# Kernel tuning notes

Hardware: AMD Instinct MI355X
Metric: run time of the kernel (lower is better)

The kernel has to match this reference:

```python
import jax, jax.numpy as jnp
import numpy as np

REG_MAX = 16
BOX_W = 7.5
OBJ_W = 1.0
TOPK = 10
EPS = 1e-7


def dfl_decode(x, reg_max):
    # x: [B, 4*reg_max, N] -> expected value of per-side distribution -> [B, N, 4] (xyxy)
    B, C, N = x.shape
    x = x.reshape(B, 4, reg_max, N)
    p = jax.nn.softmax(x, axis=2)
    proj = jnp.arange(reg_max, dtype=x.dtype)
    return jnp.einsum('bkrn,r->bnk', p, proj)


def bbox_ciou(b1, b2):
    # b1: [B,N,1,4], b2: [B,1,M,4], xyxy -> [B,N,M]
    x11, y11, x12, y12 = b1[..., 0], b1[..., 1], b1[..., 2], b1[..., 3]
    x21, y21, x22, y22 = b2[..., 0], b2[..., 1], b2[..., 2], b2[..., 3]
    w1, h1 = x12 - x11, y12 - y11
    w2, h2 = x22 - x21, y22 - y21
    iw = jnp.clip(jnp.minimum(x12, x22) - jnp.maximum(x11, x21), 0.0)
    ih = jnp.clip(jnp.minimum(y12, y22) - jnp.maximum(y11, y21), 0.0)
    inter = iw * ih
    union = w1 * h1 + w2 * h2 - inter + EPS
    iou = inter / union
    cw = jnp.maximum(x12, x22) - jnp.minimum(x11, x21)
    ch = jnp.maximum(y12, y22) - jnp.minimum(y11, y21)
    c2 = cw * cw + ch * ch + EPS
    rho2 = ((x21 + x22 - x11 - x12) ** 2 + (y21 + y22 - y11 - y12) ** 2) * 0.25
    v = (4.0 / (np.pi ** 2)) * (jnp.arctan(w2 / (h2 + EPS)) - jnp.arctan(w1 / (h1 + EPS))) ** 2
    alpha = jax.lax.stop_gradient(v / (v - iou + 1.0 + EPS))
    return iou - rho2 / c2 - alpha * v


def setup_inputs() -> dict:
    key = jax.random.key(0)
    k1, k2, k3, k4 = jax.random.split(key, 4)
    B, N, M = 8, 34000, 64
    boxes = jax.random.normal(k1, (B, 4 * REG_MAX, N), dtype=jnp.float32)
    scores = jax.random.normal(k2, (B, N), dtype=jnp.float32)
    # GT boxes: valid xyxy in roughly the same [0, reg_max) range as decoded preds
    xy = jax.random.uniform(k3, (B, M, 2), dtype=jnp.float32) * 11.0
    wh = jax.random.uniform(k4, (B, M, 2), dtype=jnp.float32) * 4.0 + 0.5
    targets = jnp.concatenate([xy, xy + wh], axis=-1)
    return {'boxes': boxes, 'scores': scores, 'targets': targets}


def reference(boxes, scores, targets):
    B, N = scores.shape
    M = targets.shape[1]
    pb = dfl_decode(boxes, REG_MAX)                     # [B,N,4]
    ciou = bbox_ciou(pb[:, :, None, :], targets[:, None, :, :])  # [B,N,M]
    k = min(TOPK, N)
    topv, topi = jax.lax.top_k(jnp.swapaxes(ciou, 1, 2), k)      # [B,M,k] over anchors
    valid = topv > 0.0
    vals = jnp.where(valid, topv, 0.0)

    def per_batch(idx, val, vld):
        flat_i = idx.reshape(-1)
        iou_t = jnp.zeros((N,), val.dtype).at[flat_i].max(val.reshape(-1))
        pos = jnp.zeros((N,), bool).at[flat_i].max(vld.reshape(-1))
        return iou_t, pos

    iou_target, pos = jax.vmap(per_batch)(topi, vals, valid)     # [B,N]
    posf = pos.astype(iou_target.dtype)
    npos = posf.sum(axis=1)
    box_per = jnp.where(npos > 0,
                        ((1.0 - iou_target) * posf).sum(axis=1) / jnp.maximum(npos, 1.0),
                        0.0)
    box_loss = box_per.sum()
    # BCEWithLogits (mean over anchors), summed over batch
    bce = jnp.maximum(scores, 0.0) - scores * iou_target + jnp.log1p(jnp.exp(-jnp.abs(scores)))
    obj_loss = bce.mean(axis=1).sum()
    total = (BOX_W * box_loss + OBJ_W * obj_loss) / B
    return total, box_loss, obj_loss
```

## Files before the change

### kernel.cpp

```cpp
#include <hip/hip_runtime.h>
#include <math.h>

#define BQ 8
#define MQ 64
#define REGMAX 16
#define KTOP 10
#define CH 4
#define EPSQ 1e-7f
#define SSEG 4
#define TRIG 256
#define CBUF (TRIG + SSEG * 256 + 16)

__device__ __forceinline__ float frcp(float x) { return __builtin_amdgcn_rcpf(x); }

#define ST_CNT 32
#define ST_BYTES 256

__global__ __launch_bounds__(256) void decode_kernel(
    const float* __restrict__ boxes, const float* __restrict__ scores,
    float4* __restrict__ pbc, float2* __restrict__ atc,
    unsigned int* __restrict__ iou_bits, float* __restrict__ state,
    int N, int bpb) {
  const int tid = threadIdx.x;
  const int b = blockIdx.x / bpb;
  const int a0 = (blockIdx.x - b * bpb) * 256;
  float* acc = state;
  int* cnt = (int*)(state + ST_CNT);

  __shared__ float s_ex[4 * 256];
  __shared__ float4 s_v4[256];
  __shared__ float2 s_ai[256];
  __shared__ float r0[256];
  __shared__ int s_cnt, s_base;
  if (tid == 0) s_cnt = 0;

  const int g = tid >> 6;
  const int l = tid & 63;
  const int na = a0 + l * 4;
  if (na + 3 < N) {
    float4 X[REGMAX];
    const size_t rowbase = ((size_t)b * 4 * REGMAX + g * REGMAX) * N + na;
#pragma unroll
    for (int r = 0; r < REGMAX; ++r)
      X[r] = *(const float4*)&boxes[rowbase + (size_t)r * N];
    const float* xf = (const float*)X;
    float ev[4];
#pragma unroll
    for (int a = 0; a < 4; ++a) {
      float mx = xf[a];
#pragma unroll
      for (int r = 1; r < REGMAX; ++r) mx = fmaxf(mx, xf[r * 4 + a]);
      float s = 0.f, ws = 0.f;
#pragma unroll
      for (int r = 0; r < REGMAX; ++r) {
        float e = __expf(xf[r * 4 + a] - mx);
        s += e;
        ws += (float)r * e;
      }
      ev[a] = ws * frcp(s);
    }
    *(float4*)&s_ex[g * 256 + l * 4] = make_float4(ev[0], ev[1], ev[2], ev[3]);
  }
  __syncthreads();

  const int n = a0 + tid;
  float bce0 = 0.f;
  if (n < N) {
    const size_t i = (size_t)b * N + n;
    iou_bits[i] = 0u;
    float sc = scores[i];
    bce0 = fmaxf(sc, 0.f) + log1pf(__expf(-fabsf(sc)));
    float x1 = s_ex[0 * 256 + tid], y1 = s_ex[1 * 256 + tid];
    float x2 = s_ex[2 * 256 + tid], y2 = s_ex[3 * 256 + tid];
    float w1 = x2 - x1, h1 = y2 - y1;
    if (w1 > 0.f && h1 > 0.f) {
      int slot = atomicAdd(&s_cnt, 1);
      s_v4[slot] = make_float4(x1, y1, x2, y2);
      s_ai[slot] = make_float2(atanf(w1 * frcp(h1 + EPSQ)), __int_as_float(n));
    }
  }
  r0[tid] = bce0;
  __syncthreads();
  const int bc = s_cnt;
  if (tid == 0) s_base = atomicAdd(&cnt[b], bc);
  for (int s = 128; s > 0; s >>= 1) {
    if (tid < s) r0[tid] += r0[tid + s];
    __syncthreads();
  }
  if (tid == 0) atomicAdd(&acc[b * 4 + 2], r0[0]);
  const int basei = s_base;
  for (int sl = tid; sl < bc; sl += 256) {
    pbc[(size_t)b * N + basei + sl] = s_v4[sl];
    atc[(size_t)b * N + basei + sl] = s_ai[sl];
  }
}

__device__ __forceinline__ void select_top10(
    float* s_bv, int* s_bi, float* s_winv, int* s_wini,
    int* s_cnt, float* s_sthr, int c, int tid) {
  if (tid < 64) {
    for (int r = 0; r < KTOP; ++r) {
      float bv = 0.f;
      int bs = 0xffff;
      for (int sl = tid; sl < c; sl += 64) {
        float v = s_bv[sl];
        if (v > bv) { bv = v; bs = sl; }
      }
      unsigned long long key =
          ((unsigned long long)__float_as_uint(bv) << 32) | (unsigned int)bs;
#pragma unroll
      for (int d = 1; d < 64; d <<= 1) {
        unsigned long long o = __shfl_xor(key, d, 64);
        if (o > key) key = o;
      }
      if (tid == 0) {
        float wv = __uint_as_float((unsigned int)(key >> 32));
        int ws = (int)(key & 0xffffu);
        s_winv[r] = wv;
        if (wv > 0.f && ws != 0xffff) {
          s_wini[r] = s_bi[ws];
          s_bv[ws] = 0.f;
        } else {
          s_wini[r] = 0;
        }
      }
    }
    if (tid < KTOP) { s_bv[tid] = s_winv[tid]; s_bi[tid] = s_wini[tid]; }
    if (tid == 0) { *s_cnt = KTOP; *s_sthr = s_winv[KTOP - 1]; }
  }
}

__global__ __launch_bounds__(256) void topk1_kernel(
    const float4* __restrict__ pbc, const float2* __restrict__ atc,
    const float* __restrict__ targets, float* __restrict__ cand_v,
    int* __restrict__ cand_i, const float* __restrict__ state, int N) {
  const int blk = blockIdx.x;
  const int chunk = blk & (CH - 1);
  const int bm = blk >> 2;
  const int b = bm >> 6;
  const int m = bm & 63;
  const int tid = threadIdx.x;
  const int* cnt = (const int*)(state + ST_CNT);

  __shared__ float s_bv[CBUF];
  __shared__ int s_bi[CBUF];
  __shared__ float s_winv[KTOP];
  __shared__ int s_wini[KTOP];
  __shared__ int s_cnt;
  __shared__ float s_sthr;
  if (tid == 0) { s_cnt = 0; s_sthr = 0.f; }
  __syncthreads();

  const float4 t = ((const float4*)targets)[b * MQ + m];
  const float x21 = t.x, y21 = t.y, x22 = t.z, y22 = t.w;
  const float w2 = x22 - x21, h2 = y22 - y21;
  const float atan_t = atanf(w2 * frcp(h2 + EPSQ));
  const float area2 = w2 * h2;
  const float sumx2 = x21 + x22, sumy2 = y21 + y22;
  const float CPI = 4.0f / (float)(M_PI * M_PI);

  const int cntb = cnt[b];
  const int cch = (cntb + CH - 1) / CH;
  const int j0 = chunk * cch;
  const int j1 = min(cntb, j0 + cch);
  float sthr = 0.f;
  const float4* pbb = pbc + (size_t)b * N;
  const float2* pab = atc + (size_t)b * N;

  for (int basei = j0; basei < j1; basei += SSEG * 256) {
#pragma unroll
    for (int s = 0; s < SSEG; ++s) {
      int j = basei + s * 256 + tid;
      if (j < j1) {
        float4 p = pbb[j];
        float2 ai = pab[j];
        float x11 = p.x, y11 = p.y, x12 = p.z, y12 = p.w;
        float w1 = x12 - x11, h1 = y12 - y11;
        float iw = fmaxf(fminf(x12, x22) - fmaxf(x11, x21), 0.f);
        float ih = fmaxf(fminf(y12, y22) - fmaxf(y11, y21), 0.f);
        float inter = iw * ih;
        float uni = w1 * h1 + area2 - inter + EPSQ;
        float iou = inter * frcp(uni);
        float cw = fmaxf(x12, x22) - fminf(x11, x21);
        float ch = fmaxf(y12, y22) - fminf(y11, y21);
        float c2 = cw * cw + ch * ch + EPSQ;
        float dx = sumx2 - x11 - x12;
        float dy = sumy2 - y11 - y12;
        float rho2 = (dx * dx + dy * dy) * 0.25f;
        float da = atan_t - ai.x;
        float v = CPI * da * da;
        float alpha = v * frcp(v - iou + 1.f + EPSQ);
        float ciou = iou - rho2 * frcp(c2) - alpha * v;
        if (ciou > sthr) {
          int slot = atomicAdd(&s_cnt, 1);
          s_bv[slot] = ciou;
          s_bi[slot] = __float_as_int(ai.y);
        }
      }
    }
    __syncthreads();
    int c = s_cnt;
    __syncthreads();
    if (c > TRIG) {
      select_top10(s_bv, s_bi, s_winv, s_wini, &s_cnt, &s_sthr, c, tid);
      __syncthreads();
    }
    sthr = s_sthr;
  }

  int c = s_cnt;
  if (c > KTOP) {
    select_top10(s_bv, s_bi, s_winv, s_wini, &s_cnt, &s_sthr, c, tid);
    __syncthreads();
    c = KTOP;
  }
  if (tid < KTOP) {
    cand_v[(bm * CH + chunk) * KTOP + tid] = (tid < c) ? s_bv[tid] : 0.f;
    cand_i[(bm * CH + chunk) * KTOP + tid] = (tid < c) ? s_bi[tid] : 0;
  }
}

__global__ __launch_bounds__(64) void topk2_kernel(
    const float* __restrict__ cand_v, const int* __restrict__ cand_i,
    const float* __restrict__ scores, unsigned int* __restrict__ iou_bits,
    float* __restrict__ state, int N) {
  const int bm = blockIdx.x;
  const int b = bm >> 6;
  const int tid = threadIdx.x;
  float* acc = state;
  const int NC = CH * KTOP;
  __shared__ float mv[NC];
  __shared__ int mi[NC];
  if (tid < NC) {
    mv[tid] = cand_v[bm * NC + tid];
    mi[tid] = cand_i[bm * NC + tid];
  }
  __syncthreads();
  if (tid < NC) {
    float v = mv[tid];
    if (v > 0.f) {
      int rank = 0;
#pragma unroll
      for (int i2 = 0; i2 < NC; ++i2)
        rank += (mv[i2] > v) || (mv[i2] == v && i2 < tid);
      if (rank < KTOP) {
        int ix = mi[tid];
        unsigned int vb = __float_as_uint(v);
        unsigned int old = atomicMax(&iou_bits[(size_t)b * N + ix], vb);
        if (old < vb) {
          float vold = __uint_as_float(old);
          bool was = (old != 0u);
          atomicAdd(&acc[b * 4 + 0], was ? (vold - v) : (1.f - v));
          if (!was) atomicAdd(&acc[b * 4 + 1], 1.f);
          atomicAdd(&acc[b * 4 + 2], -scores[(size_t)b * N + ix] * (v - vold));
        }
      }
    }
  }
}

__global__ void finalize_kernel(const float* __restrict__ acc,
                                float* __restrict__ out, int N) {
  if (threadIdx.x == 0 && blockIdx.x == 0) {
    float box = 0.f, obj = 0.f;
    for (int bb = 0; bb < BQ; ++bb) {
      float sb = acc[bb * 4 + 0];
      float np = acc[bb * 4 + 1];
      float sc = acc[bb * 4 + 2];
      box += (np > 0.f) ? sb / fmaxf(np, 1.f) : 0.f;
      obj += sc / (float)N;
    }
    out[0] = (7.5f * box + obj) / (float)BQ;
    out[1] = box;
    out[2] = obj;
  }
}

extern "C" void kernel_launch(void* const* d_in, const int* in_sizes, int n_in,
                              void* d_out, int out_size, void* d_ws, size_t ws_size,
                              hipStream_t stream) {
  const float* boxes = (const float*)d_in[0];
  const float* scores = (const float*)d_in[1];
  const float* targets = (const float*)d_in[2];
  float* out = (float*)d_out;
  const int N = in_sizes[1] / BQ;

  char* ws = (char*)d_ws;
  size_t pbc_bytes = (size_t)BQ * N * sizeof(float4);
  size_t atc_bytes = (size_t)BQ * N * sizeof(float2);
  size_t iou_bytes = (size_t)BQ * N * sizeof(unsigned int);
  size_t cand_bytes = (size_t)BQ * MQ * CH * KTOP * sizeof(float);

  float4* pbc = (float4*)ws;                   ws += pbc_bytes;
  float2* atc = (float2*)ws;                   ws += atc_bytes;
  unsigned int* iou_bits = (unsigned int*)ws;  ws += iou_bytes;
  float* cand_v = (float*)ws;                  ws += cand_bytes;
  int* cand_i = (int*)ws;                      ws += cand_bytes;
  float* state = (float*)ws;

  hipMemsetAsync(state, 0, ST_BYTES, stream);

  const int bpb = (N + 255) / 256;
  decode_kernel<<<BQ * bpb, 256, 0, stream>>>(boxes, scores, pbc, atc,
                                              iou_bits, state, N, bpb);
  topk1_kernel<<<BQ * MQ * CH, 256, 0, stream>>>(pbc, atc, targets, cand_v,
                                                 cand_i, state, N);
  topk2_kernel<<<BQ * MQ, 64, 0, stream>>>(cand_v, cand_i, scores, iou_bits,
                                           state, N);
  finalize_kernel<<<1, 64, 0, stream>>>(state, out, N);
}
```

Measured before the change: 142.1 us.

## Fuse decode with per-block CIoU top-10 and merge per-target candidates

Folds the CIoU evaluation into the decode kernel. Each block holds its surviving anchors in shared memory, and each lane (one per target) keeps a register-resident sorted top-10 over one quarter of the block's anchors. The four per-wave lists are merged and written as per-block candidates, and a second kernel reduces the bpb*10 candidates per target with shared-memory selection. This removes the compacted box buffers written to global memory, their re-reading by the 2048 top-k blocks, and one kernel launch. In exchange it adds a large candidate array and a merge that scans about 1330 candidates per target. The register insertion sort is serial per lane.

```diff
diff --git a/kernel.cpp b/kernel.cpp
--- a/kernel.cpp
+++ b/kernel.cpp
@@ -5,41 +5,38 @@
 #define MQ 64
 #define REGMAX 16
 #define KTOP 10
-#define CH 4
 #define EPSQ 1e-7f
-#define SSEG 4
-#define TRIG 256
-#define CBUF (TRIG + SSEG * 256 + 16)
+#define MBUF 1344
 
 __device__ __forceinline__ float frcp(float x) { return __builtin_amdgcn_rcpf(x); }
 
-#define ST_CNT 32
 #define ST_BYTES 256
 
-__global__ __launch_bounds__(256) void decode_kernel(
+__global__ __launch_bounds__(256) void decode_topk_kernel(
     const float* __restrict__ boxes, const float* __restrict__ scores,
-    float4* __restrict__ pbc, float2* __restrict__ atc,
-    unsigned int* __restrict__ iou_bits, float* __restrict__ state,
-    int N, int bpb) {
+    const float* __restrict__ targets, unsigned int* __restrict__ iou_bits,
+    uint2* __restrict__ cand, float* __restrict__ acc, int N, int bpb) {
   const int tid = threadIdx.x;
   const int b = blockIdx.x / bpb;
-  const int a0 = (blockIdx.x - b * bpb) * 256;
-  float* acc = state;
-  int* cnt = (int*)(state + ST_CNT);
+  const int blk = blockIdx.x - b * bpb;
+  const int a0 = blk * 256;
+  const int w = tid >> 6;
+  const int l = tid & 63;
 
   __shared__ float s_ex[4 * 256];
-  __shared__ float4 s_v4[256];
-  __shared__ float2 s_ai[256];
-  __shared__ float r0[256];
-  __shared__ int s_cnt, s_base;
-  if (tid == 0) s_cnt = 0;
-
-  const int g = tid >> 6;
-  const int l = tid & 63;
+  __shared__ float4 s_sv[256];
+  __shared__ float s_at[256];
+  __shared__ int s_ix[256];
+  __shared__ float s_hv[4 * MQ * KTOP];
+  __shared__ int s_hi[4 * MQ * KTOP];
+  __shared__ int s_cnt;
+  __shared__ float s_bce;
+  if (tid == 0) { s_cnt = 0; s_bce = 0.f; }
+
   const int na = a0 + l * 4;
   if (na + 3 < N) {
     float4 X[REGMAX];
-    const size_t rowbase = ((size_t)b * 4 * REGMAX + g * REGMAX) * N + na;
+    const size_t rowbase = ((size_t)b * 4 * REGMAX + w * REGMAX) * (size_t)N + na;
 #pragma unroll
     for (int r = 0; r < REGMAX; ++r)
       X[r] = *(const float4*)&boxes[rowbase + (size_t)r * N];
@@ -59,7 +56,7 @@
       }
       ev[a] = ws * frcp(s);
     }
-    *(float4*)&s_ex[g * 256 + l * 4] = make_float4(ev[0], ev[1], ev[2], ev[3]);
+    *(float4*)&s_ex[w * 256 + l * 4] = make_float4(ev[0], ev[1], ev[2], ev[3]);
   }
   __syncthreads();
 
@@ -70,34 +67,114 @@
     iou_bits[i] = 0u;
     float sc = scores[i];
     bce0 = fmaxf(sc, 0.f) + log1pf(__expf(-fabsf(sc)));
-    float x1 = s_ex[0 * 256 + tid], y1 = s_ex[1 * 256 + tid];
-    float x2 = s_ex[2 * 256 + tid], y2 = s_ex[3 * 256 + tid];
+    float x1 = s_ex[tid], y1 = s_ex[256 + tid];
+    float x2 = s_ex[512 + tid], y2 = s_ex[768 + tid];
     float w1 = x2 - x1, h1 = y2 - y1;
     if (w1 > 0.f && h1 > 0.f) {
       int slot = atomicAdd(&s_cnt, 1);
-      s_v4[slot] = make_float4(x1, y1, x2, y2);
-      s_ai[slot] = make_float2(atanf(w1 * frcp(h1 + EPSQ)), __int_as_float(n));
-    }
-  }
-  r0[tid] = bce0;
-  __syncthreads();
-  const int bc = s_cnt;
-  if (tid == 0) s_base = atomicAdd(&cnt[b], bc);
-  for (int s = 128; s > 0; s >>= 1) {
-    if (tid < s) r0[tid] += r0[tid + s];
-    __syncthreads();
-  }
-  if (tid == 0) atomicAdd(&acc[b * 4 + 2], r0[0]);
-  const int basei = s_base;
-  for (int sl = tid; sl < bc; sl += 256) {
-    pbc[(size_t)b * N + basei + sl] = s_v4[sl];
-    atc[(size_t)b * N + basei + sl] = s_ai[sl];
+      s_sv[slot] = make_float4(x1, y1, x2, y2);
+      s_at[slot] = atanf(w1 * frcp(h1 + EPSQ));
+      s_ix[slot] = n;
+    }
+  }
+#pragma unroll
+  for (int d = 1; d < 64; d <<= 1) bce0 += __shfl_xor(bce0, d, 64);
+  if (l == 0) atomicAdd(&s_bce, bce0);
+  __syncthreads();
+  const int nsurv = s_cnt;
+  if (tid == 0) atomicAdd(&acc[b * 4 + 2], s_bce);
+
+  const float4 t = ((const float4*)targets)[b * MQ + l];
+  const float x21 = t.x, y21 = t.y, x22 = t.z, y22 = t.w;
+  const float w2 = x22 - x21, h2 = y22 - y21;
+  const float atan_t = atanf(w2 * frcp(h2 + EPSQ));
+  const float area2 = w2 * h2, sumx2 = x21 + x22, sumy2 = y21 + y22;
+  const float CPI = 4.0f / (float)(M_PI * M_PI);
+
+  float hv0 = 0.f, hv1 = 0.f, hv2 = 0.f, hv3 = 0.f, hv4 = 0.f;
+  float hv5 = 0.f, hv6 = 0.f, hv7 = 0.f, hv8 = 0.f, hv9 = 0.f;
+  int hi0 = 0, hi1 = 0, hi2 = 0, hi3 = 0, hi4 = 0;
+  int hi5 = 0, hi6 = 0, hi7 = 0, hi8 = 0, hi9 = 0;
+
+  const int qlen = (nsurv + 3) >> 2;
+  const int j0 = w * qlen;
+  const int j1 = min(nsurv, j0 + qlen);
+  for (int j = j0; j < j1; ++j) {
+    float4 p = s_sv[j];
+    float pa = s_at[j];
+    int ixj = s_ix[j];
+    float x11 = p.x, y11 = p.y, x12 = p.z, y12 = p.w;
+    float w1 = x12 - x11, h1 = y12 - y11;
+    float iw = fmaxf(fminf(x12, x22) - fmaxf(x11, x21), 0.f);
+    float ih = fmaxf(fminf(y12, y22) - fmaxf(y11, y21), 0.f);
+    float inter = iw * ih;
+    float uni = w1 * h1 + area2 - inter + EPSQ;
+    float iou = inter * frcp(uni);
+    float cw = fmaxf(x12, x22) - fminf(x11, x21);
+    float ch = fmaxf(y12, y22) - fminf(y11, y21);
+    float c2 = cw * cw + ch * ch + EPSQ;
+    float dx = sumx2 - x11 - x12;
+    float dy = sumy2 - y11 - y12;
+    float rho2 = (dx * dx + dy * dy) * 0.25f;
+    float da = atan_t - pa;
+    float v = CPI * da * da;
+    float alpha = v * frcp(v - iou + 1.f + EPSQ);
+    float ciou = iou - rho2 * frcp(c2) - alpha * v;
+    if (ciou > hv9) {
+      float cv = ciou;
+      int ci = ixj;
+#define INS(vk, ik)                         \
+  {                                         \
+    bool gt = cv > vk;                      \
+    float tv_ = vk; int ti_ = ik;           \
+    vk = gt ? cv : vk; ik = gt ? ci : ik;   \
+    cv = gt ? tv_ : cv; ci = gt ? ti_ : ci; \
+  }
+      INS(hv0, hi0) INS(hv1, hi1) INS(hv2, hi2) INS(hv3, hi3) INS(hv4, hi4)
+      INS(hv5, hi5) INS(hv6, hi6) INS(hv7, hi7) INS(hv8, hi8) INS(hv9, hi9)
+#undef INS
+    }
+  }
+  const int hb = (w * MQ + l) * KTOP;
+  s_hv[hb + 0] = hv0; s_hi[hb + 0] = hi0;
+  s_hv[hb + 1] = hv1; s_hi[hb + 1] = hi1;
+  s_hv[hb + 2] = hv2; s_hi[hb + 2] = hi2;
+  s_hv[hb + 3] = hv3; s_hi[hb + 3] = hi3;
+  s_hv[hb + 4] = hv4; s_hi[hb + 4] = hi4;
+  s_hv[hb + 5] = hv5; s_hi[hb + 5] = hi5;
+  s_hv[hb + 6] = hv6; s_hi[hb + 6] = hi6;
+  s_hv[hb + 7] = hv7; s_hi[hb + 7] = hi7;
+  s_hv[hb + 8] = hv8; s_hi[hb + 8] = hi8;
+  s_hv[hb + 9] = hv9; s_hi[hb + 9] = hi9;
+  __syncthreads();
+
+  if (w == 0) {
+    const int m = l;
+    int p0 = 0, p1 = 0, p2 = 0, p3 = 0;
+    const size_t obase = (((size_t)(b * MQ + m)) * bpb + blk) * KTOP;
+    for (int r = 0; r < KTOP; ++r) {
+      float c0 = s_hv[(0 * MQ + m) * KTOP + p0];
+      float c1 = s_hv[(1 * MQ + m) * KTOP + p1];
+      float c2m = s_hv[(2 * MQ + m) * KTOP + p2];
+      float c3 = s_hv[(3 * MQ + m) * KTOP + p3];
+      float best = c0; int bw = 0;
+      if (c1 > best) { best = c1; bw = 1; }
+      if (c2m > best) { best = c2m; bw = 2; }
+      if (c3 > best) { best = c3; bw = 3; }
+      int psel = (bw == 0) ? p0 : (bw == 1) ? p1 : (bw == 2) ? p2 : p3;
+      int bidx = s_hi[(bw * MQ + m) * KTOP + psel];
+      cand[obase + r] = make_uint2(__float_as_uint(best), (unsigned)bidx);
+      if (bw == 0) p0 = min(p0 + 1, KTOP - 1);
+      else if (bw == 1) p1 = min(p1 + 1, KTOP - 1);
+      else if (bw == 2) p2 = min(p2 + 1, KTOP - 1);
+      else p3 = min(p3 + 1, KTOP - 1);
+    }
   }
 }
 
 __device__ __forceinline__ void select_top10(
     float* s_bv, int* s_bi, float* s_winv, int* s_wini,
-    int* s_cnt, float* s_sthr, int c, int tid) {
+    int* s_cnt, int c, int tid) {
   if (tid < 64) {
     for (int r = 0; r < KTOP; ++r) {
       float bv = 0.f;
@@ -126,134 +203,56 @@
       }
     }
     if (tid < KTOP) { s_bv[tid] = s_winv[tid]; s_bi[tid] = s_wini[tid]; }
-    if (tid == 0) { *s_cnt = KTOP; *s_sthr = s_winv[KTOP - 1]; }
-  }
-}
-
-__global__ __launch_bounds__(256) void topk1_kernel(
-    const float4* __restrict__ pbc, const float2* __restrict__ atc,
-    const float* __restrict__ targets, float* __restrict__ cand_v,
-    int* __restrict__ cand_i, const float* __restrict__ state, int N) {
-  const int blk = blockIdx.x;
-  const int chunk = blk & (CH - 1);
-  const int bm = blk >> 2;
+    if (tid == 0) *s_cnt = KTOP;
+  }
+}
+
+__global__ __launch_bounds__(256) void merge_kernel(
+    const uint2* __restrict__ cand, const float* __restrict__ scores,
+    unsigned int* __restrict__ iou_bits, float* __restrict__ acc,
+    int N, int bpb) {
+  const int bm = blockIdx.x;
   const int b = bm >> 6;
-  const int m = bm & 63;
   const int tid = threadIdx.x;
-  const int* cnt = (const int*)(state + ST_CNT);
-
-  __shared__ float s_bv[CBUF];
-  __shared__ int s_bi[CBUF];
+  const int NC = bpb * KTOP;
+
+  __shared__ float s_bv[MBUF];
+  __shared__ int s_bi[MBUF];
   __shared__ float s_winv[KTOP];
   __shared__ int s_wini[KTOP];
   __shared__ int s_cnt;
-  __shared__ float s_sthr;
-  if (tid == 0) { s_cnt = 0; s_sthr = 0.f; }
-  __syncthreads();
-
-  const float4 t = ((const float4*)targets)[b * MQ + m];
-  const float x21 = t.x, y21 = t.y, x22 = t.z, y22 = t.w;
-  const float w2 = x22 - x21, h2 = y22 - y21;
-  const float atan_t = atanf(w2 * frcp(h2 + EPSQ));
-  const float area2 = w2 * h2;
-  const float sumx2 = x21 + x22, sumy2 = y21 + y22;
-  const float CPI = 4.0f / (float)(M_PI * M_PI);
-
-  const int cntb = cnt[b];
-  const int cch = (cntb + CH - 1) / CH;
-  const int j0 = chunk * cch;
-  const int j1 = min(cntb, j0 + cch);
-  float sthr = 0.f;
-  const float4* pbb = pbc + (size_t)b * N;
-  const float2* pab = atc + (size_t)b * N;
-
-  for (int basei = j0; basei < j1; basei += SSEG * 256) {
-#pragma unroll
-    for (int s = 0; s < SSEG; ++s) {
-      int j = basei + s * 256 + tid;
-      if (j < j1) {
-        float4 p = pbb[j];
-        float2 ai = pab[j];
-        float x11 = p.x, y11 = p.y, x12 = p.z, y12 = p.w;
-        float w1 = x12 - x11, h1 = y12 - y11;
-        float iw = fmaxf(fminf(x12, x22) - fmaxf(x11, x21), 0.f);
-        float ih = fmaxf(fminf(y12, y22) - fmaxf(y11, y21), 0.f);
-        float inter = iw * ih;
-        float uni = w1 * h1 + area2 - inter + EPSQ;
-        float iou = inter * frcp(uni);
-        float cw = fmaxf(x12, x22) - fminf(x11, x21);
-        float ch = fmaxf(y12, y22) - fminf(y11, y21);
-        float c2 = cw * cw + ch * ch + EPSQ;
-        float dx = sumx2 - x11 - x12;
-        float dy = sumy2 - y11 - y12;
-        float rho2 = (dx * dx + dy * dy) * 0.25f;
-        float da = atan_t - ai.x;
-        float v = CPI * da * da;
-        float alpha = v * frcp(v - iou + 1.f + EPSQ);
-        float ciou = iou - rho2 * frcp(c2) - alpha * v;
-        if (ciou > sthr) {
-          int slot = atomicAdd(&s_cnt, 1);
-          s_bv[slot] = ciou;
-          s_bi[slot] = __float_as_int(ai.y);
-        }
-      }
-    }
-    __syncthreads();
-    int c = s_cnt;
-    __syncthreads();
-    if (c > TRIG) {
-      select_top10(s_bv, s_bi, s_winv, s_wini, &s_cnt, &s_sthr, c, tid);
-      __syncthreads();
-    }
-    sthr = s_sthr;
-  }
-
-  int c = s_cnt;
+  if (tid == 0) s_cnt = 0;
+  __syncthreads();
+
+  const uint2* base = cand + (size_t)bm * NC;
+  for (int k = tid; k < NC; k += 256) {
+    uint2 e = base[k];
+    float v = __uint_as_float(e.x);
+    if (v > 0.f) {
+      int slot = atomicAdd(&s_cnt, 1);
+      if (slot < MBUF) { s_bv[slot] = v; s_bi[slot] = (int)e.y; }
+    }
+  }
+  __syncthreads();
+  int c = min(s_cnt, MBUF);
+  __syncthreads();
   if (c > KTOP) {
-    select_top10(s_bv, s_bi, s_winv, s_wini, &s_cnt, &s_sthr, c, tid);
+    select_top10(s_bv, s_bi, s_winv, s_wini, &s_cnt, c, tid);
     __syncthreads();
     c = KTOP;
   }
-  if (tid < KTOP) {
-    cand_v[(bm * CH + chunk) * KTOP + tid] = (tid < c) ? s_bv[tid] : 0.f;
-    cand_i[(bm * CH + chunk) * KTOP + tid] = (tid < c) ? s_bi[tid] : 0;
-  }
-}
-
-__global__ __launch_bounds__(64) void topk2_kernel(
-    const float* __restrict__ cand_v, const int* __restrict__ cand_i,
-    const float* __restrict__ scores, unsigned int* __restrict__ iou_bits,
-    float* __restrict__ state, int N) {
-  const int bm = blockIdx.x;
-  const int b = bm >> 6;
-  const int tid = threadIdx.x;
-  float* acc = state;
-  const int NC = CH * KTOP;
-  __shared__ float mv[NC];
-  __shared__ int mi[NC];
-  if (tid < NC) {
-    mv[tid] = cand_v[bm * NC + tid];
-    mi[tid] = cand_i[bm * NC + tid];
-  }
-  __syncthreads();
-  if (tid < NC) {
-    float v = mv[tid];
+  if (tid < KTOP && tid < c) {
+    float v = s_bv[tid];
     if (v > 0.f) {
-      int rank = 0;
-#pragma unroll
-      for (int i2 = 0; i2 < NC; ++i2)
-        rank += (mv[i2] > v) || (mv[i2] == v && i2 < tid);
-      if (rank < KTOP) {
-        int ix = mi[tid];
-        unsigned int vb = __float_as_uint(v);
-        unsigned int old = atomicMax(&iou_bits[(size_t)b * N + ix], vb);
-        if (old < vb) {
-          float vold = __uint_as_float(old);
-          bool was = (old != 0u);
-          atomicAdd(&acc[b * 4 + 0], was ? (vold - v) : (1.f - v));
-          if (!was) atomicAdd(&acc[b * 4 + 1], 1.f);
-          atomicAdd(&acc[b * 4 + 2], -scores[(size_t)b * N + ix] * (v - vold));
-        }
+      int ix = s_bi[tid];
+      unsigned int vb = __float_as_uint(v);
+      unsigned int old = atomicMax(&iou_bits[(size_t)b * N + ix], vb);
+      if (old < vb) {
+        float vold = __uint_as_float(old);
+        bool was = (old != 0u);
+        atomicAdd(&acc[b * 4 + 0], was ? (vold - v) : (1.f - v));
+        if (!was) atomicAdd(&acc[b * 4 + 1], 1.f);
+        atomicAdd(&acc[b * 4 + 2], -scores[(size_t)b * N + ix] * (v - vold));
       }
     }
   }
@@ -285,27 +284,20 @@
   float* out = (float*)d_out;
   const int N = in_sizes[1] / BQ;
 
+  const int bpb = (N + 255) / 256;
+
   char* ws = (char*)d_ws;
-  size_t pbc_bytes = (size_t)BQ * N * sizeof(float4);
-  size_t atc_bytes = (size_t)BQ * N * sizeof(float2);
+  size_t cand_bytes = (size_t)BQ * MQ * bpb * KTOP * sizeof(uint2);
   size_t iou_bytes = (size_t)BQ * N * sizeof(unsigned int);
-  size_t cand_bytes = (size_t)BQ * MQ * CH * KTOP * sizeof(float);
-
-  float4* pbc = (float4*)ws;                   ws += pbc_bytes;
-  float2* atc = (float2*)ws;                   ws += atc_bytes;
+
+  uint2* cand = (uint2*)ws;                    ws += cand_bytes;
   unsigned int* iou_bits = (unsigned int*)ws;  ws += iou_bytes;
-  float* cand_v = (float*)ws;                  ws += cand_bytes;
-  int* cand_i = (int*)ws;                      ws += cand_bytes;
   float* state = (float*)ws;
 
   hipMemsetAsync(state, 0, ST_BYTES, stream);
 
-  const int bpb = (N + 255) / 256;
-  decode_kernel<<<BQ * bpb, 256, 0, stream>>>(boxes, scores, pbc, atc,
-                                              iou_bits, state, N, bpb);
-  topk1_kernel<<<BQ * MQ * CH, 256, 0, stream>>>(pbc, atc, targets, cand_v,
-                                                 cand_i, state, N);
-  topk2_kernel<<<BQ * MQ, 64, 0, stream>>>(cand_v, cand_i, scores, iou_bits,
-                                           state, N);
+  decode_topk_kernel<<<BQ * bpb, 256, 0, stream>>>(boxes, scores, targets,
+                                                   iou_bits, cand, state, N, bpb);
+  merge_kernel<<<BQ * MQ, 256, 0, stream>>>(cand, scores, iou_bits, state, N, bpb);
   finalize_kernel<<<1, 64, 0, stream>>>(state, out, N);
 }
```

Result: no change. 139.5 us (-1.8%).
